# Optimization experiments

Hardware: AMD Instinct MI355X
Metric: run time of the kernel (lower is better)

## Reference

```python
import jax, jax.numpy as jnp
import numpy as np
import math

BS, S, D_IN, D_OUT, RANK = 4, 2048, 4096, 4096, 128
BASE_LR = 0.01
EPS = 1e-6
SQRT_IN = math.sqrt(D_IN)  # scalar_scaler


def setup_inputs() -> dict:
    key = jax.random.key(0)
    ks = jax.random.split(key, 8)
    return {
        "x": jax.random.normal(ks[0], (BS, S, D_IN), dtype=jnp.float32),
        "log_lr": jax.random.normal(ks[1], (RANK, D_IN), dtype=jnp.float32) * 0.01,
        "state": jax.random.normal(ks[2], (BS, RANK, D_IN), dtype=jnp.float32) * 0.02,
        "grad_buffer": jax.random.normal(ks[3], (BS, RANK, D_IN), dtype=jnp.float32) * 0.01,
        "w_bsp": jax.random.normal(ks[4], (RANK, D_IN), dtype=jnp.float32) * 0.02,
        "w_out": jax.random.normal(ks[5], (D_OUT, RANK), dtype=jnp.float32) * 0.02,
        "w_lin": jax.random.normal(ks[6], (D_OUT, D_IN), dtype=jnp.float32) * 0.02,
        "b_lin": jnp.zeros((D_OUT,), dtype=jnp.float32),
    }


def reference(x, log_lr, state, grad_buffer, w_bsp, w_out, w_lin, b_lin):
    # lr = base_lr * exp(log_lr * sqrt(in_features))  -> [rank, in]
    lr = BASE_LR * jnp.exp(log_lr * SQRT_IN)
    # s = lr[None] * state  -> [bs, rank, in]; state is detached in the original
    s = lr[None] * state
    # z = einsum('boi,bsi->bso', s, x)  -> [bs, seq, rank]
    z = jnp.einsum("bri,bsi->bsr", s, x)
    # FoItttFunction.apply is identity on z in the forward
    # z + base_state_proj(x)
    z = z + jnp.einsum("bsi,ri->bsr", x, w_bsp)
    # out_proj(z) + linear(x)
    y = jnp.einsum("bsr,or->bso", z, w_out) + jnp.einsum("bsi,oi->bso", x, w_lin) + b_lin
    return y
```

## Files before the change

kernel.cpp:

```cpp
#include <hip/hip_runtime.h>
#include <hip/hip_bf16.h>

typedef __attribute__((ext_vector_type(8))) short bf16x8;
typedef __attribute__((ext_vector_type(4))) float f32x4;

#define DEVI static __device__ __forceinline__

constexpr int BS = 4, SEQ = 2048, DIN = 4096, DOUT = 4096, RANK = 128;
constexpr int MTOT = BS * SEQ;

DEVI unsigned short f2bf(float f) {
  __hip_bfloat16 h = __float2bfloat16(f);
  return __builtin_bit_cast(unsigned short, h);
}


__global__ void cast_bf16_kernel(const float* __restrict__ src,
                                 unsigned short* __restrict__ dst, int n4) {
  int i = blockIdx.x * blockDim.x + threadIdx.x;
  int stride = gridDim.x * blockDim.x;
  for (; i < n4; i += stride) {
    float4 v = reinterpret_cast<const float4*>(src)[i];
    ushort4 o;
    o.x = f2bf(v.x); o.y = f2bf(v.y); o.z = f2bf(v.z); o.w = f2bf(v.w);
    reinterpret_cast<ushort4*>(dst)[i] = o;
  }
}

__global__ void prep_m_kernel(const float* __restrict__ log_lr,
                              const float* __restrict__ state,
                              const float* __restrict__ w_bsp,
                              unsigned short* __restrict__ m_bf) {
  const int n4 = BS * RANK * DIN / 4;
  int i = blockIdx.x * blockDim.x + threadIdx.x;
  int stride = gridDim.x * blockDim.x;
  for (; i < n4; i += stride) {
    int ri4 = (i * 4) % (RANK * DIN) / 4;
    float4 ll = reinterpret_cast<const float4*>(log_lr)[ri4];
    float4 wb = reinterpret_cast<const float4*>(w_bsp)[ri4];
    float4 st = reinterpret_cast<const float4*>(state)[i];
    ushort4 o;
    o.x = f2bf(0.01f * __expf(ll.x * 64.0f) * st.x + wb.x);
    o.y = f2bf(0.01f * __expf(ll.y * 64.0f) * st.y + wb.y);
    o.z = f2bf(0.01f * __expf(ll.z * 64.0f) * st.z + wb.z);
    o.w = f2bf(0.01f * __expf(ll.w * 64.0f) * st.w + wb.w);
    reinterpret_cast<ushort4*>(m_bf)[i] = o;
  }
}


DEVI void gload16(const void* g, void* l) {
  __builtin_amdgcn_global_load_lds(
      (const __attribute__((address_space(1))) void*)g,
      (__attribute__((address_space(3))) void*)l, 16, 0, 0);
}

template <int ROWS>
DEVI void stage_tile(const char* gbase, int ldBytes, char* lds) {
  const int lane = threadIdx.x & 63;
  const int wave = threadIdx.x >> 6;
  constexpr int CHUNKS = ROWS / 16;
  constexpr int CPW = CHUNKS / 4;
  const int colByte = (lane & 3) << 4;
  const int rowInChunk = lane >> 2;
#pragma unroll
  for (int c = 0; c < CPW; ++c) {
    int chunk = wave * CPW + c;
    int row = chunk * 16 + rowInChunk;
    gload16(gbase + (size_t)row * ldBytes + colByte, lds + chunk * 1024);
  }
}

template <int F>
DEVI void compute_tile(const char* lA, const char* lB, f32x4 (&acc)[F][F]) {
  const int lane = threadIdx.x & 63;
  const int wave = threadIdx.x >> 6;
  const int wr = wave >> 1, wc = wave & 1;
  const int kByte = (lane >> 4) * 16;
  const int rsel = lane & 15;
  bf16x8 a[F], b[F];
#pragma unroll
  for (int mi = 0; mi < F; ++mi) {
    int row = wr * (F * 16) + mi * 16 + rsel;
    a[mi] = *reinterpret_cast<const bf16x8*>(lA + row * 64 + kByte);
  }
#pragma unroll
  for (int ni = 0; ni < F; ++ni) {
    int row = wc * (F * 16) + ni * 16 + rsel;
    b[ni] = *reinterpret_cast<const bf16x8*>(lB + row * 64 + kByte);
  }
#pragma unroll
  for (int mi = 0; mi < F; ++mi)
#pragma unroll
    for (int ni = 0; ni < F; ++ni)
      acc[mi][ni] =
          __builtin_amdgcn_mfma_f32_16x16x32_bf16(a[mi], b[ni], acc[mi][ni], 0, 0, 0);
}

template <int KS>
__global__ __launch_bounds__(256) void z_gemm_splitk(
    const unsigned short* __restrict__ xbf, const unsigned short* __restrict__ mbf,
    float* __restrict__ zpart) {
  int bid = blockIdx.x;
  int ksl = bid & (KS - 1);
  int rest = bid / KS;
  int nt = rest & 1, mt = rest >> 1;
  int row0 = mt * 64;
  int batch = row0 >> 11;
  int kbase = ksl * (DIN / KS);
  const char* xb = (const char*)(xbf + (size_t)row0 * DIN + kbase);
  const char* mb = (const char*)(mbf + ((size_t)batch * RANK + nt * 64) * DIN + kbase);
  __shared__ __align__(16) char lA[2][64 * 64];
  __shared__ __align__(16) char lB[2][64 * 64];
  f32x4 acc[2][2] = {};
  constexpr int NT = DIN / KS / 32;
  stage_tile<64>(xb, DIN * 2, lA[0]);
  stage_tile<64>(mb, DIN * 2, lB[0]);
  for (int t = 0; t < NT; ++t) {
    __syncthreads();
    if (t + 1 < NT) {
      stage_tile<64>(xb + (t + 1) * 64, DIN * 2, lA[(t + 1) & 1]);
      stage_tile<64>(mb + (t + 1) * 64, DIN * 2, lB[(t + 1) & 1]);
    }
    compute_tile<2>(lA[t & 1], lB[t & 1], acc);
  }
  const int lane = threadIdx.x & 63;
  const int wave = threadIdx.x >> 6;
  const int wr = wave >> 1, wc = wave & 1;
#pragma unroll
  for (int mi = 0; mi < 2; ++mi)
#pragma unroll
    for (int ni = 0; ni < 2; ++ni) {
      int c = nt * 64 + wc * 32 + ni * 16 + (lane & 15);
      int r0 = row0 + wr * 32 + mi * 16 + (lane >> 4) * 4;
#pragma unroll
      for (int j = 0; j < 4; ++j)
        zpart[((size_t)ksl * MTOT + r0 + j) * RANK + c] = acc[mi][ni][j];
    }
}

template <int KS>
__global__ void z_reduce_kernel(const float* __restrict__ zpart,
                                unsigned short* __restrict__ zbf) {
  const int n4 = MTOT * RANK / 4;
  int i = blockIdx.x * blockDim.x + threadIdx.x;
  if (i >= n4) return;
  float4 s = reinterpret_cast<const float4*>(zpart)[i];
#pragma unroll
  for (int k = 1; k < KS; ++k) {
    float4 v = reinterpret_cast<const float4*>(zpart)[(size_t)k * n4 + i];
    s.x += v.x; s.y += v.y; s.z += v.z; s.w += v.w;
  }
  ushort4 o;
  o.x = f2bf(s.x); o.y = f2bf(s.y); o.z = f2bf(s.z); o.w = f2bf(s.w);
  reinterpret_cast<ushort4*>(zbf)[i] = o;
}

__global__ __launch_bounds__(256) void z_gemm_kernel(
    const unsigned short* __restrict__ xbf, const unsigned short* __restrict__ mbf,
    unsigned short* __restrict__ zbf) {
  int mt = blockIdx.x >> 1, nt = blockIdx.x & 1;
  int row0 = mt * 64;
  int batch = row0 >> 11;
  const char* xb = (const char*)(xbf + (size_t)row0 * DIN);
  const char* mb = (const char*)(mbf + ((size_t)batch * RANK + nt * 64) * DIN);
  __shared__ __align__(16) char lA[2][64 * 64];
  __shared__ __align__(16) char lB[2][64 * 64];
  f32x4 acc[2][2] = {};
  constexpr int NT = DIN / 32;
  stage_tile<64>(xb, DIN * 2, lA[0]);
  stage_tile<64>(mb, DIN * 2, lB[0]);
  for (int t = 0; t < NT; ++t) {
    __syncthreads();
    if (t + 1 < NT) {
      stage_tile<64>(xb + (t + 1) * 64, DIN * 2, lA[(t + 1) & 1]);
      stage_tile<64>(mb + (t + 1) * 64, DIN * 2, lB[(t + 1) & 1]);
    }
    compute_tile<2>(lA[t & 1], lB[t & 1], acc);
  }
  const int lane = threadIdx.x & 63;
  const int wave = threadIdx.x >> 6;
  const int wr = wave >> 1, wc = wave & 1;
#pragma unroll
  for (int mi = 0; mi < 2; ++mi)
#pragma unroll
    for (int ni = 0; ni < 2; ++ni) {
      int c = nt * 64 + wc * 32 + ni * 16 + (lane & 15);
      int r0 = row0 + wr * 32 + mi * 16 + (lane >> 4) * 4;
#pragma unroll
      for (int j = 0; j < 4; ++j)
        zbf[(size_t)(r0 + j) * RANK + c] = f2bf(acc[mi][ni][j]);
    }
}


struct MainCtx {
  const char* lds;
  int wr, wc, rsel, kgrp, xorv;
};

DEVI const bf16x8* lda_frag(const MainCtx& c, int d, int mi, int ks) {
  int col = ((ks * 64) + c.kgrp * 16) ^ c.xorv;
  return reinterpret_cast<const bf16x8*>(
      c.lds + d * 32768 + c.wr * 16384 + mi * 2048 + c.rsel * 128 + col);
}
DEVI const bf16x8* ldb_frag(const MainCtx& c, int d, int ni, int ks) {
  int col = ((ks * 64) + c.kgrp * 16) ^ c.xorv;
  return reinterpret_cast<const bf16x8*>(
      c.lds + 65536 + d * 32768 + (c.wc >> 1) * 16384 + (c.wc & 1) * 8192 +
      ni * 2048 + c.rsel * 128 + col);
}

template <int D, int Q, class STG>
DEVI void phase_body(const MainCtx& c, f32x4 (&acc)[8][4], bf16x8 (&bfr)[4][2],
                     STG&& stg) {
  bf16x8 a00 = *lda_frag(c, D, 2 * Q, 0);
  bf16x8 a01 = *lda_frag(c, D, 2 * Q, 1);
  bf16x8 a10 = *lda_frag(c, D, 2 * Q + 1, 0);
  bf16x8 a11 = *lda_frag(c, D, 2 * Q + 1, 1);
  if (Q == 0) {
#pragma unroll
    for (int ni = 0; ni < 4; ++ni) {
      bfr[ni][0] = *ldb_frag(c, D, ni, 0);
      bfr[ni][1] = *ldb_frag(c, D, ni, 1);
    }
  }
  stg();
  __builtin_amdgcn_s_barrier();
  asm volatile("s_waitcnt lgkmcnt(0)" ::: "memory");
  __builtin_amdgcn_s_setprio(1);
#pragma unroll
  for (int ni = 0; ni < 4; ++ni) {
    acc[2 * Q][ni] = __builtin_amdgcn_mfma_f32_16x16x32_bf16(a00, bfr[ni][0], acc[2 * Q][ni], 0, 0, 0);
    acc[2 * Q + 1][ni] = __builtin_amdgcn_mfma_f32_16x16x32_bf16(a10, bfr[ni][0], acc[2 * Q + 1][ni], 0, 0, 0);
  }
#pragma unroll
  for (int ni = 0; ni < 4; ++ni) {
    acc[2 * Q][ni] = __builtin_amdgcn_mfma_f32_16x16x32_bf16(a01, bfr[ni][1], acc[2 * Q][ni], 0, 0, 0);
    acc[2 * Q + 1][ni] = __builtin_amdgcn_mfma_f32_16x16x32_bf16(a11, bfr[ni][1], acc[2 * Q + 1][ni], 0, 0, 0);
  }
  __builtin_amdgcn_s_setprio(0);
  asm volatile("s_waitcnt vmcnt(4)" ::: "memory");
  __builtin_amdgcn_s_barrier();
}

__global__ __launch_bounds__(512, 2) void main_gemm_8p(
    const unsigned short* __restrict__ xbf, const unsigned short* __restrict__ wlbf,
    const unsigned short* __restrict__ zbf, const unsigned short* __restrict__ wobf,
    const float* __restrict__ b_lin, float* __restrict__ out) {
  __shared__ __align__(16) char lds[131072];

  const int tid = threadIdx.x;
  const int lane = tid & 63, wave = tid >> 6;

  int bid = blockIdx.x;
  int swz = (bid & 7) * 64 + (bid >> 3);
  int mt = swz >> 4, nt = swz & 15;
  const int row0 = mt * 256, col0 = nt * 256;

  const char* xb = (const char*)(xbf + (size_t)row0 * DIN);
  const char* wb = (const char*)(wlbf + (size_t)col0 * DIN);
  const char* zb = (const char*)(zbf + (size_t)row0 * RANK);
  const char* ob = (const char*)(wobf + (size_t)col0 * RANK);

  const int srow8 = lane >> 3;
  const int scolS = ((lane & 7) ^ srow8) << 4;
  const int chunk0 = wave * 2;

  auto stage = [&](const char* gbase, int ld, int ldsOff) {
    gload16(gbase + (size_t)(chunk0 * 8 + srow8) * ld + scolS,
            (void*)&lds[ldsOff + chunk0 * 1024]);
    gload16(gbase + (size_t)(chunk0 * 8 + 8 + srow8) * ld + scolS,
            (void*)&lds[ldsOff + chunk0 * 1024 + 1024]);
  };
  auto stageA = [&](int k, int h, int d) {
    const char* g; int ld;
    if (k < 64) { g = xb + (size_t)h * 128 * (DIN * 2) + (size_t)k * 128; ld = DIN * 2; }
    else        { g = zb + (size_t)h * 128 * (RANK * 2) + (size_t)(k - 64) * 128; ld = RANK * 2; }
    stage(g, ld, d * 32768 + h * 16384);
  };
  auto stageB = [&](int k, int h, int d) {
    const char* g; int ld;
    if (k < 64) { g = wb + (size_t)h * 128 * (DIN * 2) + (size_t)k * 128; ld = DIN * 2; }
    else        { g = ob + (size_t)h * 128 * (RANK * 2) + (size_t)(k - 64) * 128; ld = RANK * 2; }
    stage(g, ld, 65536 + d * 32768 + h * 16384);
  };

  MainCtx c{lds, wave >> 2, wave & 3, lane & 15, lane >> 4, (lane & 7) << 4};

  f32x4 acc[8][4] = {};
  bf16x8 bfr[4][2];

  stageB(0, 0, 0); stageB(0, 1, 0);
  stageA(0, 0, 0); stageA(0, 1, 0);
  stageB(1, 0, 1); stageB(1, 1, 1);
  asm volatile("s_waitcnt vmcnt(4)" ::: "memory");
  __builtin_amdgcn_s_barrier();

  constexpr int NKT = 66;
  for (int j = 0; j < NKT / 2; ++j) {
    int t = 2 * j;
    int kA1 = (t + 1 < NKT - 1) ? t + 1 : NKT - 1;
    int kN2 = (t + 2 < NKT - 1) ? t + 2 : NKT - 1;
    int kB3 = (t + 3 < NKT - 1) ? t + 3 : NKT - 1;
    phase_body<0, 0>(c, acc, bfr, [&] { stageA(kA1, 0, 1); });
    phase_body<0, 1>(c, acc, bfr, [&] { stageA(kA1, 1, 1); });
    phase_body<0, 2>(c, acc, bfr, [&] { stageB(kN2, 0, 0); });
    phase_body<0, 3>(c, acc, bfr, [&] { stageB(kN2, 1, 0); });
    phase_body<1, 0>(c, acc, bfr, [&] { stageA(kN2, 0, 0); });
    phase_body<1, 1>(c, acc, bfr, [&] { stageA(kN2, 1, 0); });
    phase_body<1, 2>(c, acc, bfr, [&] { stageB(kB3, 0, 1); });
    phase_body<1, 3>(c, acc, bfr, [&] { stageB(kB3, 1, 1); });
  }
  asm volatile("s_waitcnt vmcnt(0)" ::: "memory");

  const int wr = wave >> 2, wc = wave & 3;
  const int rbase = row0 + wr * 128 + (lane >> 4) * 4;
  const int cbase = col0 + wc * 64 + (lane & 15);
#pragma unroll
  for (int mi = 0; mi < 8; ++mi)
#pragma unroll
    for (int ni = 0; ni < 4; ++ni) {
      int cc = cbase + ni * 16;
      float bv = b_lin[cc];
      int r = rbase + mi * 16;
#pragma unroll
      for (int j2 = 0; j2 < 4; ++j2)
        out[(size_t)(r + j2) * DOUT + cc] = acc[mi][ni][j2] + bv;
    }
}


extern "C" void kernel_launch(void* const* d_in, const int* in_sizes, int n_in,
                              void* d_out, int out_size, void* d_ws, size_t ws_size,
                              hipStream_t stream) {
  const float* x = (const float*)d_in[0];
  const float* log_lr = (const float*)d_in[1];
  const float* state = (const float*)d_in[2];
  const float* w_bsp = (const float*)d_in[4];
  const float* w_out = (const float*)d_in[5];
  const float* w_lin = (const float*)d_in[6];
  const float* b_lin = (const float*)d_in[7];
  float* out = (float*)d_out;

  unsigned short* xbf = (unsigned short*)d_ws;
  unsigned short* wlbf = xbf + (size_t)MTOT * DIN;
  unsigned short* wobf = wlbf + (size_t)DOUT * DIN;
  unsigned short* mbf = wobf + (size_t)DOUT * RANK;
  unsigned short* zbf = mbf + (size_t)BS * RANK * DIN;
  float* zpart = (float*)(zbf + (size_t)MTOT * RANK);
  const size_t need_split = 108003328 + 16777216;

  cast_bf16_kernel<<<2048, 256, 0, stream>>>(x, xbf, MTOT * DIN / 4);
  cast_bf16_kernel<<<2048, 256, 0, stream>>>(w_lin, wlbf, DOUT * DIN / 4);
  cast_bf16_kernel<<<512, 256, 0, stream>>>(w_out, wobf, DOUT * RANK / 4);
  prep_m_kernel<<<2048, 256, 0, stream>>>(log_lr, state, w_bsp, mbf);

  if (ws_size >= need_split) {
    z_gemm_splitk<4><<<1024, 256, 0, stream>>>(xbf, mbf, zpart);
    z_reduce_kernel<4><<<1024, 256, 0, stream>>>(zpart, zbf);
  } else {
    z_gemm_kernel<<<256, 256, 0, stream>>>(xbf, mbf, zbf);
  }

  main_gemm_8p<<<512, 512, 0, stream>>>(xbf, wlbf, zbf, wobf, b_lin, out);
}
```

Measured before the change: 563.2 us.

## Double-buffer LDS fragments in registers and reschedule global staging across phases

Result: no change. 554.4 us (-1.6%).

```diff
diff --git a/kernel.cpp b/kernel.cpp
--- a/kernel.cpp
+++ b/kernel.cpp
@@ -211,36 +211,46 @@
       ni * 2048 + c.rsel * 128 + col);
 }
 
-template <int D, int Q, class STG>
-DEVI void phase_body(const MainCtx& c, f32x4 (&acc)[8][4], bf16x8 (&bfr)[4][2],
-                     STG&& stg) {
-  bf16x8 a00 = *lda_frag(c, D, 2 * Q, 0);
-  bf16x8 a01 = *lda_frag(c, D, 2 * Q, 1);
-  bf16x8 a10 = *lda_frag(c, D, 2 * Q + 1, 0);
-  bf16x8 a11 = *lda_frag(c, D, 2 * Q + 1, 1);
-  if (Q == 0) {
-#pragma unroll
-    for (int ni = 0; ni < 4; ++ni) {
-      bfr[ni][0] = *ldb_frag(c, D, ni, 0);
-      bfr[ni][1] = *ldb_frag(c, D, ni, 1);
-    }
+template <int PH>
+struct PhaseCfg {
+  static constexpr int q = PH & 3;
+  static constexpr int mih = q & 1;
+  static constexpr int aCur = PH & 1;
+  static constexpr int aNxt = (PH + 1) & 1;
+  static constexpr int bCur = (PH >> 1) & 1;
+  static constexpr int nq = (PH + 1) & 3;
+  static constexpr int nbuf = ((PH + 1) >> 2) & 1;
+  static constexpr int nks = nq >> 1;
+  static constexpr int nmih = nq & 1;
+  static constexpr bool rdB = (PH & 1) == 1;
+  static constexpr int bNxt = ((PH + 1) >> 1) & 1;
+};
+
+template <int PH, bool VM0, class STG>
+DEVI void phase(const MainCtx& c, f32x4 (&acc)[8][4], bf16x8 (&aS)[2][4],
+                bf16x8 (&bS)[2][4], STG&& stg) {
+  using P = PhaseCfg<PH>;
+#pragma unroll
+  for (int m = 0; m < 4; ++m)
+    aS[P::aNxt][m] = *lda_frag(c, P::nbuf, P::nmih * 4 + m, P::nks);
+  if constexpr (P::rdB) {
+#pragma unroll
+    for (int ni = 0; ni < 4; ++ni)
+      bS[P::bNxt][ni] = *ldb_frag(c, P::nbuf, ni, P::nks);
   }
   stg();
-  __builtin_amdgcn_s_barrier();
-  asm volatile("s_waitcnt lgkmcnt(0)" ::: "memory");
   __builtin_amdgcn_s_setprio(1);
 #pragma unroll
-  for (int ni = 0; ni < 4; ++ni) {
-    acc[2 * Q][ni] = __builtin_amdgcn_mfma_f32_16x16x32_bf16(a00, bfr[ni][0], acc[2 * Q][ni], 0, 0, 0);
-    acc[2 * Q + 1][ni] = __builtin_amdgcn_mfma_f32_16x16x32_bf16(a10, bfr[ni][0], acc[2 * Q + 1][ni], 0, 0, 0);
-  }
-#pragma unroll
-  for (int ni = 0; ni < 4; ++ni) {
-    acc[2 * Q][ni] = __builtin_amdgcn_mfma_f32_16x16x32_bf16(a01, bfr[ni][1], acc[2 * Q][ni], 0, 0, 0);
-    acc[2 * Q + 1][ni] = __builtin_amdgcn_mfma_f32_16x16x32_bf16(a11, bfr[ni][1], acc[2 * Q + 1][ni], 0, 0, 0);
-  }
+  for (int m = 0; m < 4; ++m)
+#pragma unroll
+    for (int ni = 0; ni < 4; ++ni)
+      acc[P::mih * 4 + m][ni] = __builtin_amdgcn_mfma_f32_16x16x32_bf16(
+          aS[P::aCur][m], bS[P::bCur][ni], acc[P::mih * 4 + m][ni], 0, 0, 0);
   __builtin_amdgcn_s_setprio(0);
-  asm volatile("s_waitcnt vmcnt(4)" ::: "memory");
+  if constexpr (VM0)
+    asm volatile("s_waitcnt vmcnt(0)" ::: "memory");
+  else
+    asm volatile("" ::: "memory");
   __builtin_amdgcn_s_barrier();
 }
 
@@ -289,13 +299,17 @@
   MainCtx c{lds, wave >> 2, wave & 3, lane & 15, lane >> 4, (lane & 7) << 4};
 
   f32x4 acc[8][4] = {};
-  bf16x8 bfr[4][2];
-
+  bf16x8 aS[2][4], bS[2][4];
+
+  stageA(0, 0, 0); stageA(0, 1, 0);
   stageB(0, 0, 0); stageB(0, 1, 0);
-  stageA(0, 0, 0); stageA(0, 1, 0);
-  stageB(1, 0, 1); stageB(1, 1, 1);
-  asm volatile("s_waitcnt vmcnt(4)" ::: "memory");
+  stageB(1, 0, 1);
+  asm volatile("s_waitcnt vmcnt(2)" ::: "memory");
   __builtin_amdgcn_s_barrier();
+#pragma unroll
+  for (int m = 0; m < 4; ++m) aS[0][m] = *lda_frag(c, 0, m, 0);
+#pragma unroll
+  for (int ni = 0; ni < 4; ++ni) bS[0][ni] = *ldb_frag(c, 0, ni, 0);
 
   constexpr int NKT = 66;
   for (int j = 0; j < NKT / 2; ++j) {
@@ -303,14 +317,16 @@
     int kA1 = (t + 1 < NKT - 1) ? t + 1 : NKT - 1;
     int kN2 = (t + 2 < NKT - 1) ? t + 2 : NKT - 1;
     int kB3 = (t + 3 < NKT - 1) ? t + 3 : NKT - 1;
-    phase_body<0, 0>(c, acc, bfr, [&] { stageA(kA1, 0, 1); });
-    phase_body<0, 1>(c, acc, bfr, [&] { stageA(kA1, 1, 1); });
-    phase_body<0, 2>(c, acc, bfr, [&] { stageB(kN2, 0, 0); });
-    phase_body<0, 3>(c, acc, bfr, [&] { stageB(kN2, 1, 0); });
-    phase_body<1, 0>(c, acc, bfr, [&] { stageA(kN2, 0, 0); });
-    phase_body<1, 1>(c, acc, bfr, [&] { stageA(kN2, 1, 0); });
-    phase_body<1, 2>(c, acc, bfr, [&] { stageB(kB3, 0, 1); });
-    phase_body<1, 3>(c, acc, bfr, [&] { stageB(kB3, 1, 1); });
+    phase<0, false>(c, acc, aS, bS,
+                    [&] { stageA(kA1, 0, 1); stageA(kA1, 1, 1); stageB(kA1, 1, 1); });
+    phase<1, false>(c, acc, aS, bS, [&] {});
+    phase<2, true >(c, acc, aS, bS, [&] {});
+    phase<3, false>(c, acc, aS, bS, [&] { stageB(kN2, 0, 0); });
+    phase<4, false>(c, acc, aS, bS,
+                    [&] { stageA(kN2, 0, 0); stageA(kN2, 1, 0); stageB(kN2, 1, 0); });
+    phase<5, false>(c, acc, aS, bS, [&] {});
+    phase<6, true >(c, acc, aS, bS, [&] {});
+    phase<7, false>(c, acc, aS, bS, [&] { stageB(kB3, 0, 1); });
   }
   asm volatile("s_waitcnt vmcnt(0)" ::: "memory");
 
```
